# Kernel tuning notes

Measured on AMD Instinct MI355X. Metric: run time of the kernel, lower is better.

## Reference

```python
import jax, jax.numpy as jnp
import numpy as np

B, ES, HS, NL, NOUT, T = 16384, 64, 64, 3, 2, 128


def setup_inputs() -> dict:
    key = jax.random.key(0)
    ks = jax.random.split(key, 9)
    k = 1.0 / np.sqrt(HS)
    u = lambda kk, shape: jax.random.uniform(kk, shape, jnp.float32, -k, k)
    return {
        "agentFutureTrajEnc": jax.random.normal(ks[0], (B, ES), jnp.float32),
        "emb_w": u(ks[1], (ES, ES)),
        "emb_b": u(ks[2], (ES,)),
        "w_ih": u(ks[3], (NL, 3 * HS, ES)),
        "w_hh": u(ks[4], (NL, 3 * HS, HS)),
        "b_ih": u(ks[5], (NL, 3 * HS)),
        "b_hh": u(ks[6], (NL, 3 * HS)),
        "out_w": u(ks[7], (NOUT, HS)),
        "out_b": u(ks[8], (NOUT,)),
        "target_length": T,
        "batch_size": B,
    }


def _gru_cell(x, h, Wi, Wh, bi, bh):
    # PyTorch GRU cell math: gates ordered (r, z, n)
    gi = x @ Wi.T + bi            # (B, 3*hs)
    gh = h @ Wh.T + bh            # (B, 3*hs)
    ir, iz, inn = jnp.split(gi, 3, axis=-1)
    hr, hz, hn = jnp.split(gh, 3, axis=-1)
    r = jax.nn.sigmoid(ir + hr)
    z = jax.nn.sigmoid(iz + hz)
    n = jnp.tanh(inn + r * hn)
    return (1.0 - z) * n + z * h


def reference(agentFutureTrajEnc, emb_w, emb_b, w_ih, w_hh, b_ih, b_hh, out_w, out_b,
              target_length, batch_size):
    nl = w_ih.shape[0]
    # hidden initialized by repeating the encoding across layers: (nl, B, hs)
    h0 = jnp.broadcast_to(agentFutureTrajEnc[None], (nl,) + agentFutureTrajEnc.shape)

    def step(carry, _):
        x, h = carry                      # x: (B, es), h: (nl, B, hs)
        inp = x @ emb_w.T + emb_b         # embedding Linear(es->es)
        new_h = []
        for l in range(nl):               # small fixed layer loop
            hl = _gru_cell(inp, h[l], w_ih[l], w_hh[l], b_ih[l], b_hh[l])
            new_h.append(hl)
            inp = hl
        h = jnp.stack(new_h)              # (nl, B, hs)
        out = inp @ out_w.T + out_b       # (B, nout)
        return (h[-1], h), out            # next input is top-layer hidden

    _, outs = jax.lax.scan(step, (agentFutureTrajEnc, h0), None, length=target_length)
    return jnp.transpose(outs, (1, 0, 2))  # (B, T, nout)
```

## Files before the change

### kernel.cpp

```cpp
#include <hip/hip_runtime.h>


#define ESZ   64
#define HSZ   64
#define NLAY  3
#define TLEN  128
#define NOUTC 2
#define TILE  16
#define TILES 4
#define LDW   72
#define TB    (TILE*LDW)
#define L2E   1.44269504f

typedef _Float16 half8 __attribute__((ext_vector_type(8)));
typedef float    floatx4 __attribute__((ext_vector_type(4)));

#define MFMA(a, b, c) __builtin_amdgcn_mfma_f32_16x16x32_f16((a), (b), (c), 0, 0, 0)

__device__ __forceinline__ void wg_barrier() {
    asm volatile("s_waitcnt lgkmcnt(0)" ::: "memory");
    __builtin_amdgcn_s_barrier();
    asm volatile("" ::: "memory");
}

__global__ __launch_bounds__(768, 3) void gru_pipe(
    const float* __restrict__ enc,
    const float* __restrict__ emb_w,
    const float* __restrict__ emb_b,
    const float* __restrict__ w_ih,
    const float* __restrict__ w_hh,
    const float* __restrict__ b_ih,
    const float* __restrict__ b_hh,
    const float* __restrict__ out_w,
    const float* __restrict__ out_b,
    float* __restrict__ out)
{
    __shared__ _Float16 s_hl[NLAY * TILES * 2 * TB];

    const int tid  = threadIdx.x;
    const int wave = tid >> 6, lane = tid & 63;
    const int l = wave >> 2, g = wave & 3;
    const int q = lane >> 4, c = lane & 15;
    const int u = (g << 4) | c;
    const long wgbase = (long)blockIdx.x * (TILES * TILE);

    if (tid < 512) {
        const int row = tid >> 3, k0 = (tid & 7) << 3;
        const int j = row >> 4, rr = row & 15;
        const float* p = enc + (wgbase + row) * ESZ + k0;
        floatx4 s0 = *(const floatx4*)p;
        floatx4 s1 = *(const floatx4*)(p + 4);
        half8 v;
        #pragma unroll
        for (int x = 0; x < 4; ++x) { v[x] = (_Float16)s0[x]; v[4 + x] = (_Float16)s1[x]; }
        #pragma unroll
        for (int ly = 0; ly < NLAY; ++ly)
            *(half8*)&s_hl[((ly * TILES + j) * 2 + 1) * TB + rr * LDW + k0] = v;
    }

    auto ldw8s = [&](const float* p, float sc) {
        floatx4 a = *(const floatx4*)p, b = *(const floatx4*)(p + 4);
        half8 v;
        #pragma unroll
        for (int x = 0; x < 4; ++x) { v[x] = (_Float16)(a[x] * sc); v[4 + x] = (_Float16)(b[x] * sc); }
        return v;
    };
    half8 fR[4], fZ[4], fNi[2], fNh[2], fO[2];
    float bias0, bias1, bias2, bias3, outb = 0.f;
    if (l == 0) {
        const float* wi = w_ih;
        const float* wh = w_hh;
        floatx4 aR[4], aZ[4], aN[4];
        #pragma unroll
        for (int x = 0; x < 4; ++x) { aR[x] = {0,0,0,0}; aZ[x] = {0,0,0,0}; aN[x] = {0,0,0,0}; }
        float bR = 0.f, bZ = 0.f, bN = 0.f;
        for (int k4 = 0; k4 < 64; k4 += 4) {
            floatx4 wr4 = *(const floatx4*)(wi + (u) * 64 + k4);
            floatx4 wz4 = *(const floatx4*)(wi + (64 + u) * 64 + k4);
            floatx4 wn4 = *(const floatx4*)(wi + (128 + u) * 64 + k4);
            floatx4 be4 = *(const floatx4*)(emb_b + k4);
            #pragma unroll
            for (int kk = 0; kk < 4; ++kk) {
                const float* er = emb_w + (k4 + kk) * 64;
                floatx4 e0 = *(const floatx4*)(er + q * 8);
                floatx4 e1 = *(const floatx4*)(er + q * 8 + 4);
                floatx4 e2 = *(const floatx4*)(er + 32 + q * 8);
                floatx4 e3 = *(const floatx4*)(er + 32 + q * 8 + 4);
                const float wr = wr4[kk], wz = wz4[kk], wn = wn4[kk];
                aR[0] += wr * e0; aR[1] += wr * e1; aR[2] += wr * e2; aR[3] += wr * e3;
                aZ[0] += wz * e0; aZ[1] += wz * e1; aZ[2] += wz * e2; aZ[3] += wz * e3;
                aN[0] += wn * e0; aN[1] += wn * e1; aN[2] += wn * e2; aN[3] += wn * e3;
                bR += wr * be4[kk]; bZ += wz * be4[kk]; bN += wn * be4[kk];
            }
        }
        #pragma unroll
        for (int x = 0; x < 4; ++x) {
            fR[0][x] = (_Float16)(-L2E * aR[0][x]);   fR[0][4 + x] = (_Float16)(-L2E * aR[1][x]);
            fR[1][x] = (_Float16)(-L2E * aR[2][x]);   fR[1][4 + x] = (_Float16)(-L2E * aR[3][x]);
            fZ[0][x] = (_Float16)(-L2E * aZ[0][x]);   fZ[0][4 + x] = (_Float16)(-L2E * aZ[1][x]);
            fZ[1][x] = (_Float16)(-L2E * aZ[2][x]);   fZ[1][4 + x] = (_Float16)(-L2E * aZ[3][x]);
            fNi[0][x] = (_Float16)(2*L2E * aN[0][x]); fNi[0][4 + x] = (_Float16)(2*L2E * aN[1][x]);
            fNi[1][x] = (_Float16)(2*L2E * aN[2][x]); fNi[1][4 + x] = (_Float16)(2*L2E * aN[3][x]);
        }
        fR[2]  = ldw8s(wh + (u) * 64 + q * 8, -L2E);        fR[3]  = ldw8s(wh + (u) * 64 + 32 + q * 8, -L2E);
        fZ[2]  = ldw8s(wh + (64 + u) * 64 + q * 8, -L2E);   fZ[3]  = ldw8s(wh + (64 + u) * 64 + 32 + q * 8, -L2E);
        fNh[0] = ldw8s(wh + (128 + u) * 64 + q * 8, 2*L2E); fNh[1] = ldw8s(wh + (128 + u) * 64 + 32 + q * 8, 2*L2E);
        bias0 = -L2E * (bR + b_ih[u] + b_hh[u]);
        bias1 = -L2E * (bZ + b_ih[64 + u] + b_hh[64 + u]);
        bias2 = 2.f * L2E * (bN + b_ih[128 + u]);
        bias3 = 2.f * L2E * b_hh[128 + u];
        const int oc = (c < NOUTC) ? c : 0;
        fO[0] = ldw8s(out_w + oc * 64 + q * 8, 1.f);
        fO[1] = ldw8s(out_w + oc * 64 + 32 + q * 8, 1.f);
        outb = (c < NOUTC) ? out_b[c] : 0.f;
    } else {
        const float* wi = w_ih + l * 3 * HSZ * ESZ;
        const float* wh = w_hh + l * 3 * HSZ * ESZ;
        fR[0]  = ldw8s(wi + (u) * 64 + q * 8, -L2E);        fR[1]  = ldw8s(wi + (u) * 64 + 32 + q * 8, -L2E);
        fR[2]  = ldw8s(wh + (u) * 64 + q * 8, -L2E);        fR[3]  = ldw8s(wh + (u) * 64 + 32 + q * 8, -L2E);
        fZ[0]  = ldw8s(wi + (64 + u) * 64 + q * 8, -L2E);   fZ[1]  = ldw8s(wi + (64 + u) * 64 + 32 + q * 8, -L2E);
        fZ[2]  = ldw8s(wh + (64 + u) * 64 + q * 8, -L2E);   fZ[3]  = ldw8s(wh + (64 + u) * 64 + 32 + q * 8, -L2E);
        fNi[0] = ldw8s(wi + (128 + u) * 64 + q * 8, 2*L2E); fNi[1] = ldw8s(wi + (128 + u) * 64 + 32 + q * 8, 2*L2E);
        fNh[0] = ldw8s(wh + (128 + u) * 64 + q * 8, 2*L2E); fNh[1] = ldw8s(wh + (128 + u) * 64 + 32 + q * 8, 2*L2E);
        const int b0 = l * 3 * HSZ;
        bias0 = -L2E * (b_ih[b0 + u] + b_hh[b0 + u]);
        bias1 = -L2E * (b_ih[b0 + 64 + u] + b_hh[b0 + 64 + u]);
        bias2 = 2.f * L2E * b_ih[b0 + 128 + u];
        bias3 = 2.f * L2E * b_hh[b0 + 128 + u];
        fO[0] = fO[1] = half8{};
    }

    floatx4 carr0, carr1, carr2, carr3;
    {
        floatx4 tmp[4];
        #pragma unroll
        for (int p = 0; p < 4; ++p) {
            const int jp = (p - l) & 3;
            floatx4 hv;
            #pragma unroll
            for (int i = 0; i < 4; ++i)
                hv[i] = enc[(wgbase + jp * TILE + q * 4 + i) * ESZ + u];
            tmp[p] = hv;
        }
        carr0 = tmp[0]; carr1 = tmp[1]; carr2 = tmp[2]; carr3 = tmp[3];
    }
    const int ar = c * LDW + q * 8;
    __syncthreads();

    auto gru = [&](half8 ax0, half8 ax1, half8 ah0, half8 ah1, floatx4& carr, _Float16* hw) {
        floatx4 accr  = {bias0, bias0, bias0, bias0};
        floatx4 accz  = {bias1, bias1, bias1, bias1};
        floatx4 accni = {bias2, bias2, bias2, bias2};
        floatx4 accnh = {bias3, bias3, bias3, bias3};
        accr  = MFMA(ah0, fR[2], accr);   accr  = MFMA(ah1, fR[3], accr);
        accz  = MFMA(ah0, fZ[2], accz);   accz  = MFMA(ah1, fZ[3], accz);
        accnh = MFMA(ah0, fNh[0], accnh); accnh = MFMA(ah1, fNh[1], accnh);
        accr  = MFMA(ax0, fR[0], accr);   accr  = MFMA(ax1, fR[1], accr);
        accz  = MFMA(ax0, fZ[0], accz);   accz  = MFMA(ax1, fZ[1], accz);
        accni = MFMA(ax0, fNi[0], accni); accni = MFMA(ax1, fNi[1], accni);
        const floatx4 hold = carr;
        floatx4 hnew;
        #pragma unroll
        for (int i = 0; i < 4; ++i) {
            const float r  = __builtin_amdgcn_rcpf(1.f + __builtin_amdgcn_exp2f(accr[i]));
            const float z  = __builtin_amdgcn_rcpf(1.f + __builtin_amdgcn_exp2f(accz[i]));
            const float a  = accni[i] + r * accnh[i];
            const float n  = 1.f - 2.f * __builtin_amdgcn_rcpf(1.f + __builtin_amdgcn_exp2f(a));
            const float hv = n + z * (hold[i] - n);
            hnew[i] = hv;
            hw[(q * 4 + i) * LDW + u] = (_Float16)hv;
        }
        carr = hnew;
    };

    half8 ah0p, ah1p, ax0p{}, ax1p{};
    {
        const int jn = (0 - l) & 3;
        const int tn = (l > 0) ? -1 : 0;
        const _Float16* hb = &s_hl[((l * TILES + jn) * 2 + ((tn + 1) & 1)) * TB];
        ah0p = *(const half8*)&hb[ar];
        ah1p = *(const half8*)&hb[ar + 32];
        if (l == 0) {
            const _Float16* xb = &s_hl[((2 * TILES + jn) * 2 + ((tn + 1) & 1)) * TB];
            ax0p = *(const half8*)&xb[ar];
            ax1p = *(const half8*)&xb[ar + 32];
        }
    }

    auto phase = [&](const int js, floatx4& carr, const int s4) {
        const int j = (js - l) & 3;
        const int t = s4 - ((js < l) ? 1 : 0);
        const half8 ah0 = ah0p, ah1 = ah1p, ax0 = ax0p, ax1 = ax1p;
        {
            const int jsn = (js + 1) & 3;
            const int s4n = s4 + ((js == 3) ? 1 : 0);
            const int jn  = (jsn - l) & 3;
            const int tn  = s4n - ((jsn < l) ? 1 : 0);
            const int par = (tn + 1) & 1;
            const _Float16* hb = &s_hl[((l * TILES + jn) * 2 + par) * TB];
            ah0p = *(const half8*)&hb[ar];
            ah1p = *(const half8*)&hb[ar + 32];
            if (l == 0) {
                const _Float16* xb = &s_hl[((2 * TILES + jn) * 2 + par) * TB];
                ax0p = *(const half8*)&xb[ar];
                ax1p = *(const half8*)&xb[ar + 32];
            }
        }
        if (l == 0) {
            if (t >= 1 && g == 0) {
                floatx4 acc = {outb, outb, outb, outb};
                acc = MFMA(ax0, fO[0], acc);
                acc = MFMA(ax1, fO[1], acc);
                if (c < NOUTC) {
                    #pragma unroll
                    for (int i = 0; i < 4; ++i)
                        out[((wgbase + j * TILE + q * 4 + i) * TLEN + (t - 1)) * NOUTC + c] = acc[i];
                }
            }
            if (t < TLEN)
                gru(ax0, ax1, ah0, ah1, carr, &s_hl[((0 * TILES + j) * 2 + (t & 1)) * TB]);
        } else {
            if (t >= 0 && t < TLEN) {
                const _Float16* xb = &s_hl[(((l - 1) * TILES + j) * 2 + (t & 1)) * TB];
                half8 bx0 = *(const half8*)&xb[ar];
                half8 bx1 = *(const half8*)&xb[ar + 32];
                gru(bx0, bx1, ah0, ah1, carr, &s_hl[((l * TILES + j) * 2 + (t & 1)) * TB]);
            }
        }
        wg_barrier();
    };

    for (int s4 = 0; s4 <= TLEN; ++s4) {
        phase(0, carr0, s4);
        phase(1, carr1, s4);
        phase(2, carr2, s4);
        phase(3, carr3, s4);
    }
}

extern "C" void kernel_launch(void* const* d_in, const int* in_sizes, int n_in,
                              void* d_out, int out_size, void* d_ws, size_t ws_size,
                              hipStream_t stream) {
    (void)in_sizes; (void)n_in; (void)d_ws; (void)ws_size; (void)out_size;
    const int grid = 16384 / (TILES * TILE);
    gru_pipe<<<grid, 768, 0, stream>>>(
        (const float*)d_in[0],
        (const float*)d_in[1],
        (const float*)d_in[2],
        (const float*)d_in[3],
        (const float*)d_in[4],
        (const float*)d_in[5],
        (const float*)d_in[6],
        (const float*)d_in[7],
        (const float*)d_in[8],
        (float*)d_out);
}
```

Before: 490.2 us.

## Replace workgroup barriers with per-tile LDS flag dataflow between layer waves

```diff
diff --git a/kernel.cpp b/kernel.cpp
--- a/kernel.cpp
+++ b/kernel.cpp
@@ -3,25 +3,18 @@
 
 #define ESZ   64
 #define HSZ   64
-#define NLAY  3
 #define TLEN  128
 #define NOUTC 2
-#define TILE  16
-#define TILES 4
 #define LDW   72
-#define TB    (TILE*LDW)
+#define TB    (16*LDW)
 #define L2E   1.44269504f
 
 typedef _Float16 half8 __attribute__((ext_vector_type(8)));
+typedef _Float16 half4 __attribute__((ext_vector_type(4)));
 typedef float    floatx4 __attribute__((ext_vector_type(4)));
+typedef float    floatx2 __attribute__((ext_vector_type(2)));
 
 #define MFMA(a, b, c) __builtin_amdgcn_mfma_f32_16x16x32_f16((a), (b), (c), 0, 0, 0)
-
-__device__ __forceinline__ void wg_barrier() {
-    asm volatile("s_waitcnt lgkmcnt(0)" ::: "memory");
-    __builtin_amdgcn_s_barrier();
-    asm volatile("" ::: "memory");
-}
 
 __global__ __launch_bounds__(768, 3) void gru_pipe(
     const float* __restrict__ enc,
@@ -35,14 +28,17 @@
     const float* __restrict__ out_b,
     float* __restrict__ out)
 {
-    __shared__ _Float16 s_hl[NLAY * TILES * 2 * TB];
+    __shared__ _Float16 s_hl[3 * 4 * 2 * TB];
+    __shared__ float    s_btmp[3 * 64];
+    __shared__ int      s_flag[12];
 
     const int tid  = threadIdx.x;
     const int wave = tid >> 6, lane = tid & 63;
     const int l = wave >> 2, g = wave & 3;
     const int q = lane >> 4, c = lane & 15;
-    const int u = (g << 4) | c;
-    const long wgbase = (long)blockIdx.x * (TILES * TILE);
+    const int u  = (g << 4) | c;
+    const int u4 = (g << 4) | (q << 2);
+    const long wgbase = (long)blockIdx.x * 64;
 
     if (tid < 512) {
         const int row = tid >> 3, k0 = (tid & 7) << 3;
@@ -54,9 +50,10 @@
         #pragma unroll
         for (int x = 0; x < 4; ++x) { v[x] = (_Float16)s0[x]; v[4 + x] = (_Float16)s1[x]; }
         #pragma unroll
-        for (int ly = 0; ly < NLAY; ++ly)
-            *(half8*)&s_hl[((ly * TILES + j) * 2 + 1) * TB + rr * LDW + k0] = v;
-    }
+        for (int ly = 0; ly < 3; ++ly)
+            *(half8*)&s_hl[((ly * 4 + j) * 2 + 1) * TB + rr * LDW + k0] = v;
+    }
+    if (tid < 12) s_flag[tid] = 0;
 
     auto ldw8s = [&](const float* p, float sc) {
         floatx4 a = *(const floatx4*)p, b = *(const floatx4*)(p + 4);
@@ -66,7 +63,7 @@
         return v;
     };
     half8 fR[4], fZ[4], fNi[2], fNh[2], fO[2];
-    float bias0, bias1, bias2, bias3, outb = 0.f;
+    fO[0] = fO[1] = half8{};
     if (l == 0) {
         const float* wi = w_ih;
         const float* wh = w_hh;
@@ -105,14 +102,12 @@
         fR[2]  = ldw8s(wh + (u) * 64 + q * 8, -L2E);        fR[3]  = ldw8s(wh + (u) * 64 + 32 + q * 8, -L2E);
         fZ[2]  = ldw8s(wh + (64 + u) * 64 + q * 8, -L2E);   fZ[3]  = ldw8s(wh + (64 + u) * 64 + 32 + q * 8, -L2E);
         fNh[0] = ldw8s(wh + (128 + u) * 64 + q * 8, 2*L2E); fNh[1] = ldw8s(wh + (128 + u) * 64 + 32 + q * 8, 2*L2E);
-        bias0 = -L2E * (bR + b_ih[u] + b_hh[u]);
-        bias1 = -L2E * (bZ + b_ih[64 + u] + b_hh[64 + u]);
-        bias2 = 2.f * L2E * (bN + b_ih[128 + u]);
-        bias3 = 2.f * L2E * b_hh[128 + u];
+        if (q == 0) {
+            s_btmp[u] = bR; s_btmp[64 + u] = bZ; s_btmp[128 + u] = bN;
+        }
         const int oc = (c < NOUTC) ? c : 0;
         fO[0] = ldw8s(out_w + oc * 64 + q * 8, 1.f);
         fO[1] = ldw8s(out_w + oc * 64 + 32 + q * 8, 1.f);
-        outb = (c < NOUTC) ? out_b[c] : 0.f;
     } else {
         const float* wi = w_ih + l * 3 * HSZ * ESZ;
         const float* wh = w_hh + l * 3 * HSZ * ESZ;
@@ -122,119 +117,103 @@
         fZ[2]  = ldw8s(wh + (64 + u) * 64 + q * 8, -L2E);   fZ[3]  = ldw8s(wh + (64 + u) * 64 + 32 + q * 8, -L2E);
         fNi[0] = ldw8s(wi + (128 + u) * 64 + q * 8, 2*L2E); fNi[1] = ldw8s(wi + (128 + u) * 64 + 32 + q * 8, 2*L2E);
         fNh[0] = ldw8s(wh + (128 + u) * 64 + q * 8, 2*L2E); fNh[1] = ldw8s(wh + (128 + u) * 64 + 32 + q * 8, 2*L2E);
-        const int b0 = l * 3 * HSZ;
-        bias0 = -L2E * (b_ih[b0 + u] + b_hh[b0 + u]);
-        bias1 = -L2E * (b_ih[b0 + 64 + u] + b_hh[b0 + 64 + u]);
-        bias2 = 2.f * L2E * b_ih[b0 + 128 + u];
-        bias3 = 2.f * L2E * b_hh[b0 + 128 + u];
-        fO[0] = fO[1] = half8{};
-    }
-
-    floatx4 carr0, carr1, carr2, carr3;
-    {
-        floatx4 tmp[4];
-        #pragma unroll
-        for (int p = 0; p < 4; ++p) {
-            const int jp = (p - l) & 3;
-            floatx4 hv;
-            #pragma unroll
-            for (int i = 0; i < 4; ++i)
-                hv[i] = enc[(wgbase + jp * TILE + q * 4 + i) * ESZ + u];
-            tmp[p] = hv;
-        }
-        carr0 = tmp[0]; carr1 = tmp[1]; carr2 = tmp[2]; carr3 = tmp[3];
-    }
-    const int ar = c * LDW + q * 8;
+    }
     __syncthreads();
 
-    auto gru = [&](half8 ax0, half8 ax1, half8 ah0, half8 ah1, floatx4& carr, _Float16* hw) {
-        floatx4 accr  = {bias0, bias0, bias0, bias0};
-        floatx4 accz  = {bias1, bias1, bias1, bias1};
-        floatx4 accni = {bias2, bias2, bias2, bias2};
-        floatx4 accnh = {bias3, bias3, bias3, bias3};
-        accr  = MFMA(ah0, fR[2], accr);   accr  = MFMA(ah1, fR[3], accr);
-        accz  = MFMA(ah0, fZ[2], accz);   accz  = MFMA(ah1, fZ[3], accz);
-        accnh = MFMA(ah0, fNh[0], accnh); accnh = MFMA(ah1, fNh[1], accnh);
-        accr  = MFMA(ax0, fR[0], accr);   accr  = MFMA(ax1, fR[1], accr);
-        accz  = MFMA(ax0, fZ[0], accz);   accz  = MFMA(ax1, fZ[1], accz);
-        accni = MFMA(ax0, fNi[0], accni); accni = MFMA(ax1, fNi[1], accni);
-        const floatx4 hold = carr;
-        floatx4 hnew;
+    floatx4 bR4, bZ4, bNi4, bNh4;
+    if (l == 0) {
+        #pragma unroll
+        for (int i = 0; i < 4; ++i) {
+            bR4[i]  = -L2E * (s_btmp[u4 + i] + b_ih[u4 + i] + b_hh[u4 + i]);
+            bZ4[i]  = -L2E * (s_btmp[64 + u4 + i] + b_ih[64 + u4 + i] + b_hh[64 + u4 + i]);
+            bNi4[i] = 2.f * L2E * (s_btmp[128 + u4 + i] + b_ih[128 + u4 + i]);
+            bNh4[i] = 2.f * L2E * b_hh[128 + u4 + i];
+        }
+    } else {
+        const int b0 = l * 192;
+        floatx4 bi0 = *(const floatx4*)(b_ih + b0 + u4),       bh0 = *(const floatx4*)(b_hh + b0 + u4);
+        floatx4 bi1 = *(const floatx4*)(b_ih + b0 + 64 + u4),  bh1 = *(const floatx4*)(b_hh + b0 + 64 + u4);
+        floatx4 bi2 = *(const floatx4*)(b_ih + b0 + 128 + u4), bh2 = *(const floatx4*)(b_hh + b0 + 128 + u4);
+        #pragma unroll
+        for (int i = 0; i < 4; ++i) {
+            bR4[i]  = -L2E * (bi0[i] + bh0[i]);
+            bZ4[i]  = -L2E * (bi1[i] + bh1[i]);
+            bNi4[i] = 2.f * L2E * bi2[i];
+            bNh4[i] = 2.f * L2E * bh2[i];
+        }
+    }
+    const float ob0 = out_b[0], ob1 = out_b[1];
+
+    floatx4 ca0 = *(const floatx4*)(enc + (wgbase + 0 * 16 + c) * 64 + u4);
+    floatx4 ca1 = *(const floatx4*)(enc + (wgbase + 1 * 16 + c) * 64 + u4);
+    floatx4 ca2 = *(const floatx4*)(enc + (wgbase + 2 * 16 + c) * 64 + u4);
+    floatx4 ca3 = *(const floatx4*)(enc + (wgbase + 3 * 16 + c) * 64 + u4);
+
+    const int ar = c * LDW + (q << 3);
+    const int fh = l * 4, fx = ((l == 0) ? 2 : (l - 1)) * 4;
+
+    auto iter = [&](const int j, floatx4& carr, const int t) {
+        const int parh = (t + 1) & 1, parw = t & 1;
+        { volatile const int* f = &s_flag[fh + j]; const int tg = 4 * t; while (*f < tg) {} }
+        asm volatile("" ::: "memory");
+        const _Float16* hb = s_hl + ((fh + j) * 2 + parh) * TB;
+        half8 ah0 = *(const half8*)(hb + ar), ah1 = *(const half8*)(hb + ar + 32);
+        floatx4 accr = bR4, accz = bZ4, accni = bNi4, accnh = bNh4;
+        accr  = MFMA(fR[2], ah0, accr);   accr  = MFMA(fR[3], ah1, accr);
+        accz  = MFMA(fZ[2], ah0, accz);   accz  = MFMA(fZ[3], ah1, accz);
+        accnh = MFMA(fNh[0], ah0, accnh); accnh = MFMA(fNh[1], ah1, accnh);
+        { volatile const int* f = &s_flag[fx + j]; const int tg = (l == 0) ? 4 * t : 4 * t + 4; while (*f < tg) {} }
+        asm volatile("" ::: "memory");
+        const _Float16* xb = (l == 0) ? s_hl + ((2 * 4 + j) * 2 + parh) * TB
+                                      : s_hl + (((l - 1) * 4 + j) * 2 + parw) * TB;
+        half8 bx0 = *(const half8*)(xb + ar), bx1 = *(const half8*)(xb + ar + 32);
+        if (l == 0 && g == 0 && t >= 1) {
+            floatx4 oa = {ob0, ob1, 0.f, 0.f};
+            oa = MFMA(fO[0], bx0, oa);
+            oa = MFMA(fO[1], bx1, oa);
+            if (q == 0) {
+                const long row = wgbase + j * 16 + c;
+                *(floatx2*)(out + (row * TLEN + (t - 1)) * NOUTC) = floatx2{oa[0], oa[1]};
+            }
+        }
+        accr  = MFMA(fR[0], bx0, accr);   accr  = MFMA(fR[1], bx1, accr);
+        accz  = MFMA(fZ[0], bx0, accz);   accz  = MFMA(fZ[1], bx1, accz);
+        accni = MFMA(fNi[0], bx0, accni); accni = MFMA(fNi[1], bx1, accni);
+        half4 hv4; floatx4 hnew;
         #pragma unroll
         for (int i = 0; i < 4; ++i) {
             const float r  = __builtin_amdgcn_rcpf(1.f + __builtin_amdgcn_exp2f(accr[i]));
             const float z  = __builtin_amdgcn_rcpf(1.f + __builtin_amdgcn_exp2f(accz[i]));
             const float a  = accni[i] + r * accnh[i];
             const float n  = 1.f - 2.f * __builtin_amdgcn_rcpf(1.f + __builtin_amdgcn_exp2f(a));
-            const float hv = n + z * (hold[i] - n);
-            hnew[i] = hv;
-            hw[(q * 4 + i) * LDW + u] = (_Float16)hv;
-        }
+            const float hv = n + z * (carr[i] - n);
+            hnew[i] = hv; hv4[i] = (_Float16)hv;
+        }
+        *(half4*)(s_hl + ((fh + j) * 2 + parw) * TB + c * LDW + u4) = hv4;
         carr = hnew;
+        asm volatile("s_waitcnt lgkmcnt(0)" ::: "memory");
+        if (lane == 0) atomicAdd(&s_flag[fh + j], 1);
     };
 
-    half8 ah0p, ah1p, ax0p{}, ax1p{};
-    {
-        const int jn = (0 - l) & 3;
-        const int tn = (l > 0) ? -1 : 0;
-        const _Float16* hb = &s_hl[((l * TILES + jn) * 2 + ((tn + 1) & 1)) * TB];
-        ah0p = *(const half8*)&hb[ar];
-        ah1p = *(const half8*)&hb[ar + 32];
-        if (l == 0) {
-            const _Float16* xb = &s_hl[((2 * TILES + jn) * 2 + ((tn + 1) & 1)) * TB];
-            ax0p = *(const half8*)&xb[ar];
-            ax1p = *(const half8*)&xb[ar + 32];
-        }
-    }
-
-    auto phase = [&](const int js, floatx4& carr, const int s4) {
-        const int j = (js - l) & 3;
-        const int t = s4 - ((js < l) ? 1 : 0);
-        const half8 ah0 = ah0p, ah1 = ah1p, ax0 = ax0p, ax1 = ax1p;
-        {
-            const int jsn = (js + 1) & 3;
-            const int s4n = s4 + ((js == 3) ? 1 : 0);
-            const int jn  = (jsn - l) & 3;
-            const int tn  = s4n - ((jsn < l) ? 1 : 0);
-            const int par = (tn + 1) & 1;
-            const _Float16* hb = &s_hl[((l * TILES + jn) * 2 + par) * TB];
-            ah0p = *(const half8*)&hb[ar];
-            ah1p = *(const half8*)&hb[ar + 32];
-            if (l == 0) {
-                const _Float16* xb = &s_hl[((2 * TILES + jn) * 2 + par) * TB];
-                ax0p = *(const half8*)&xb[ar];
-                ax1p = *(const half8*)&xb[ar + 32];
+    for (int t = 0; t < TLEN; ++t) {
+        iter(0, ca0, t); iter(1, ca1, t); iter(2, ca2, t); iter(3, ca3, t);
+    }
+
+    if (l == 0 && g == 0) {
+        #pragma unroll
+        for (int j = 0; j < 4; ++j) {
+            { volatile const int* f = &s_flag[2 * 4 + j]; while (*f < 4 * TLEN) {} }
+            asm volatile("" ::: "memory");
+            const _Float16* xb = s_hl + ((2 * 4 + j) * 2 + 1) * TB;
+            half8 bx0 = *(const half8*)(xb + ar), bx1 = *(const half8*)(xb + ar + 32);
+            floatx4 oa = {ob0, ob1, 0.f, 0.f};
+            oa = MFMA(fO[0], bx0, oa);
+            oa = MFMA(fO[1], bx1, oa);
+            if (q == 0) {
+                const long row = wgbase + j * 16 + c;
+                *(floatx2*)(out + (row * TLEN + 127) * NOUTC) = floatx2{oa[0], oa[1]};
             }
         }
-        if (l == 0) {
-            if (t >= 1 && g == 0) {
-                floatx4 acc = {outb, outb, outb, outb};
-                acc = MFMA(ax0, fO[0], acc);
-                acc = MFMA(ax1, fO[1], acc);
-                if (c < NOUTC) {
-                    #pragma unroll
-                    for (int i = 0; i < 4; ++i)
-                        out[((wgbase + j * TILE + q * 4 + i) * TLEN + (t - 1)) * NOUTC + c] = acc[i];
-                }
-            }
-            if (t < TLEN)
-                gru(ax0, ax1, ah0, ah1, carr, &s_hl[((0 * TILES + j) * 2 + (t & 1)) * TB]);
-        } else {
-            if (t >= 0 && t < TLEN) {
-                const _Float16* xb = &s_hl[(((l - 1) * TILES + j) * 2 + (t & 1)) * TB];
-                half8 bx0 = *(const half8*)&xb[ar];
-                half8 bx1 = *(const half8*)&xb[ar + 32];
-                gru(bx0, bx1, ah0, ah1, carr, &s_hl[((l * TILES + j) * 2 + (t & 1)) * TB]);
-            }
-        }
-        wg_barrier();
-    };
-
-    for (int s4 = 0; s4 <= TLEN; ++s4) {
-        phase(0, carr0, s4);
-        phase(1, carr1, s4);
-        phase(2, carr2, s4);
-        phase(3, carr3, s4);
     }
 }
 
@@ -242,7 +221,7 @@
                               void* d_out, int out_size, void* d_ws, size_t ws_size,
                               hipStream_t stream) {
     (void)in_sizes; (void)n_in; (void)d_ws; (void)ws_size; (void)out_size;
-    const int grid = 16384 / (TILES * TILE);
+    const int grid = 16384 / 64;
     gru_pipe<<<grid, 768, 0, stream>>>(
         (const float*)d_in[0],
         (const float*)d_in[1],
```

Result: faster. 448.3 us (-8.5%).
